# Kernel optimization log

Hardware: AMD Instinct MI355X
Metric: run time of the kernel (lower is better)

## Reference

```python
import jax, jax.numpy as jnp
import numpy as np

B, S, DIM, H = 2, 2048, 1536, 12
HD = DIM // H  # 128
EPS = 1e-6


def setup_inputs() -> dict:
    key = jax.random.key(0)
    ks = jax.random.split(key, 6)
    x = jax.random.normal(ks[0], (B, S, DIM), dtype=jnp.float32)
    # RoPE rotation as (cos, sin) pairs: shape [S, 1, HD//2, 2]
    inv = 1.0 / (10000.0 ** (np.arange(0, HD, 2, dtype=np.float32) / HD))
    ang = np.arange(S, dtype=np.float32)[:, None] * inv[None, :]  # [S, HD//2]
    freqs = jnp.asarray(np.stack([np.cos(ang), np.sin(ang)], axis=-1))[:, None, :, :]
    def lin(k):
        return jax.random.normal(k, (DIM, DIM), dtype=jnp.float32) * 0.02
    wq, wk, wv, wo = lin(ks[1]), lin(ks[2]), lin(ks[3]), lin(ks[4])
    zb = jnp.zeros((DIM,), dtype=jnp.float32)
    ones = jnp.ones((DIM,), dtype=jnp.float32)
    return dict(x=x, freqs=freqs,
                wq=wq, bq=zb, wk=wk, bk=zb, wv=wv, bv=zb, wo=wo, bo=zb,
                gq=ones, gk=ones, timestep=500)


def reference(x, freqs, wq, bq, wk, bk, wv, bv, wo, bo, gq, gk, timestep):
    b, s, dim = x.shape

    def rms(z, g):
        zf = z.astype(jnp.float32)
        n = zf * jax.lax.rsqrt(jnp.mean(zf * zf, axis=-1, keepdims=True) + EPS)
        return n.astype(z.dtype) * g

    def rope(t):
        # [b,s,dim] -> [b,s,H,HD//2,2] pairs; complex multiply by freqs
        tp = t.reshape(b, s, H, HD // 2, 2)
        tr, ti = tp[..., 0], tp[..., 1]
        fr = freqs[None, ..., 0]  # [1,s,1,HD//2] broadcasts over batch & heads
        fi = freqs[None, ..., 1]
        out = jnp.stack([tr * fr - ti * fi, tr * fi + ti * fr], axis=-1)
        return out.reshape(b, s, dim)

    q = rope(rms(x @ wq.T + bq, gq))
    k = rope(rms(x @ wk.T + bk, gk))
    v = x @ wv.T + bv

    qh = q.reshape(b, s, H, HD).transpose(0, 2, 1, 3)
    kh = k.reshape(b, s, H, HD).transpose(0, 2, 1, 3)
    vh = v.reshape(b, s, H, HD).transpose(0, 2, 1, 3)
    scores = jnp.einsum('bhqd,bhkd->bhqk', qh, kh) / np.float32(np.sqrt(HD))
    attn = jax.nn.softmax(scores, axis=-1)
    out = jnp.einsum('bhqk,bhkd->bhqd', attn, vh)
    out = out.transpose(0, 2, 1, 3).reshape(b, s, dim)
    return out @ wo.T + bo
```

## Files before the change

kernel.cpp:

```cpp
#include <hip/hip_runtime.h>
#include <hip/hip_bf16.h>


#define BQ  2
#define SQ  2048
#define DIMQ 1536
#define HQ  12
#define HDQ 128
#define MTOK 4096
#define KDIM 1536

typedef __attribute__((ext_vector_type(8))) short short8;
typedef __attribute__((ext_vector_type(4))) float f32x4;
typedef __attribute__((ext_vector_type(16))) float f32x16;
typedef __attribute__((ext_vector_type(8))) unsigned short u16x8;

typedef __attribute__((address_space(1))) const void global_cvoid;
typedef __attribute__((address_space(3))) void lds_void;

__device__ __forceinline__ float bf2f(unsigned int u) {
    return __uint_as_float(u << 16);
}
__device__ __forceinline__ unsigned short f2bf(float f) {
    unsigned int u = __float_as_uint(f);
    u += 0x7fffu + ((u >> 16) & 1u);
    return (unsigned short)(u >> 16);
}
__device__ __forceinline__ void gload_lds16(const void* g, void* l) {
    __builtin_amdgcn_global_load_lds((global_cvoid*)g, (lds_void*)l, 16, 0, 0);
}
__device__ __forceinline__ unsigned int cvtpk_bf16(float lo, float hi) {
    unsigned int r;
    asm("v_cvt_pk_bf16_f32 %0, %1, %2" : "=v"(r) : "v"(lo), "v"(hi));
    return r;
}

#define VMCNT(n) asm volatile("s_waitcnt vmcnt(" #n ")" ::: "memory")
#define MEMFENCE() asm volatile("" ::: "memory")
#define BARRIER() do { asm volatile("" ::: "memory"); \
                       __builtin_amdgcn_s_barrier();  \
                       asm volatile("" ::: "memory"); } while (0)

__global__ __launch_bounds__(256)
void cast_all(const float* __restrict__ x,
              const float* __restrict__ wq, const float* __restrict__ wk,
              const float* __restrict__ wv, const float* __restrict__ wo,
              unsigned short* __restrict__ Xb,
              unsigned short* __restrict__ Wqkv,
              unsigned short* __restrict__ Wob)
{
    const int NX = 1572864, NW = 589824;
    int i = blockIdx.x * blockDim.x + threadIdx.x;
    int stride = gridDim.x * blockDim.x;
    for (; i < NX + 4 * NW; i += stride) {
        const float* s; unsigned short* d; int off;
        if (i < NX) { s = x; d = Xb; off = i; }
        else {
            int j = i - NX;
            int seg = j / NW;
            off = j - seg * NW;
            s = (seg == 0) ? wq : (seg == 1) ? wk : (seg == 2) ? wv : wo;
            d = (seg < 3) ? (Wqkv + seg * 2359296) : Wob;
        }
        float4 v = ((const float4*)s)[off];
        unsigned short a = f2bf(v.x), b = f2bf(v.y), c = f2bf(v.z), e = f2bf(v.w);
        unsigned int lo = (unsigned int)a | ((unsigned int)b << 16);
        unsigned int hi = (unsigned int)c | ((unsigned int)e << 16);
        ((uint2*)d)[off] = make_uint2(lo, hi);
    }
}

template<int MODE>
__global__ __launch_bounds__(256)
void gemm_bt(const unsigned short* __restrict__ A,
             const unsigned short* __restrict__ Bm,
             unsigned short* __restrict__ oQ,
             unsigned short* __restrict__ oK,
             unsigned short* __restrict__ oV,
             const float* __restrict__ biasq,
             const float* __restrict__ biask,
             const float* __restrict__ biasv,
             float* __restrict__ oF,
             const float* __restrict__ biaso)
{
    __shared__ char smem[32768];
    const int m0 = blockIdx.x * 128;
    const int n0 = blockIdx.y * 128;
    const int t = threadIdx.x;
    const int lane = t & 63;
    const int wid = t >> 6;
    const int wr = (wid >> 1) * 64;
    const int wc = (wid & 1) * 64;
    const int lr = lane & 15;
    const int lk = lane >> 4;

    f32x4 acc[4][4] = {};

    #pragma unroll
    for (int i = 0; i < 2; ++i) {
        const int off = i * 4096 + wid * 1024 + lane * 16;
        const int r = off >> 6;
        const int c = (off >> 4) & 3;
        const int csw = (c ^ (r & 3)) << 3;
        gload_lds16(A + (size_t)(m0 + r) * KDIM + csw,
                    smem + i * 4096 + wid * 1024);
        gload_lds16(Bm + (size_t)(n0 + r) * KDIM + csw,
                    smem + 16384 + i * 4096 + wid * 1024);
    }

    #pragma unroll 1
    for (int s = 0; s < KDIM / 32; ++s) {
        const int cb = s & 1;
        if (s + 1 < KDIM / 32) {
            const int kt = (s + 1) * 32;
            #pragma unroll
            for (int i = 0; i < 2; ++i) {
                const int off = i * 4096 + wid * 1024 + lane * 16;
                const int r = off >> 6;
                const int c = (off >> 4) & 3;
                const int csw = (c ^ (r & 3)) << 3;
                gload_lds16(A + (size_t)(m0 + r) * KDIM + kt + csw,
                            smem + (cb ^ 1) * 8192 + i * 4096 + wid * 1024);
                gload_lds16(Bm + (size_t)(n0 + r) * KDIM + kt + csw,
                            smem + 16384 + (cb ^ 1) * 8192 + i * 4096 + wid * 1024);
            }
            VMCNT(4);
        } else {
            VMCNT(0);
        }
        BARRIER();

        short8 af[4], bf[4];
        #pragma unroll
        for (int mi = 0; mi < 4; ++mi) {
            int row = wr + mi * 16 + lr;
            int ch = lk ^ (row & 3);
            af[mi] = *(const short8*)(smem + cb * 8192 + row * 64 + ch * 16);
        }
        #pragma unroll
        for (int ni = 0; ni < 4; ++ni) {
            int row = wc + ni * 16 + lr;
            int ch = lk ^ (row & 3);
            bf[ni] = *(const short8*)(smem + 16384 + cb * 8192 + row * 64 + ch * 16);
        }
        #pragma unroll
        for (int mi = 0; mi < 4; ++mi)
            #pragma unroll
            for (int ni = 0; ni < 4; ++ni)
                acc[mi][ni] = __builtin_amdgcn_mfma_f32_16x16x32_bf16(
                    af[mi], bf[ni], acc[mi][ni], 0, 0, 0);

        BARRIER();
    }

    if (MODE == 0) {
        const int seg = n0 / 1536;
        const int nl0 = n0 - seg * 1536;
        if (seg < 2) {
            unsigned short* op = (seg == 0) ? oQ : oK;
            const float* bp = (seg == 0) ? biasq : biask;
            #pragma unroll
            for (int mi = 0; mi < 4; ++mi)
                #pragma unroll
                for (int ni = 0; ni < 4; ++ni)
                    #pragma unroll
                    for (int j = 0; j < 4; ++j) {
                        int row = m0 + wr + mi * 16 + lk * 4 + j;
                        int col = nl0 + wc + ni * 16 + lr;
                        op[(size_t)row * 1536 + col] = f2bf(acc[mi][ni][j] + bp[col]);
                    }
        } else {
            #pragma unroll
            for (int mi = 0; mi < 4; ++mi)
                #pragma unroll
                for (int ni = 0; ni < 4; ++ni)
                    #pragma unroll
                    for (int j = 0; j < 4; ++j) {
                        int sl = wr + mi * 16 + lk * 4 + j;
                        int dl = wc + ni * 16 + lr;
                        unsigned short val = f2bf(acc[mi][ni][j] + biasv[nl0 + dl]);
                        *(unsigned short*)(smem + dl * 256 +
                            ((((sl >> 3) ^ (dl & 15))) << 4) + (sl & 7) * 2) = val;
                    }
            BARRIER();
            const int h = nl0 >> 7;
            const int bb = m0 >> 11;
            const int sseq0 = m0 & 2047;
            const int bh = bb * HQ + h;
            #pragma unroll
            for (int p = 0; p < 8; ++p) {
                int d = wid * 32 + p * 4 + lk;
                int sc = lr;
                u16x8 v = *(const u16x8*)(smem + d * 256 + ((sc ^ (d & 15)) << 4));
                *(u16x8*)(oV + (size_t)(bh * HDQ + d) * SQ + sseq0 + sc * 8) = v;
            }
        }
    } else {
        #pragma unroll
        for (int mi = 0; mi < 4; ++mi)
            #pragma unroll
            for (int ni = 0; ni < 4; ++ni)
                #pragma unroll
                for (int j = 0; j < 4; ++j) {
                    int row = m0 + wr + mi * 16 + lk * 4 + j;
                    int col = n0 + wc + ni * 16 + lr;
                    oF[(size_t)row * 1536 + col] = acc[mi][ni][j] + biaso[col];
                }
    }
}

__global__ __launch_bounds__(256)
void rmsnorm_rope(unsigned short* __restrict__ Qb,
                  unsigned short* __restrict__ Kb,
                  const float* __restrict__ gq,
                  const float* __restrict__ gk,
                  const float* __restrict__ freqs)
{
    unsigned short* T = blockIdx.y ? Kb : Qb;
    const float* g = blockIdx.y ? gk : gq;
    const int token = blockIdx.x;
    const int s = token & (SQ - 1);
    unsigned int* row = (unsigned int*)(T + (size_t)token * DIMQ);
    const int t = threadIdx.x;
    const int lane = t & 63, wid = t >> 6;

    float pr[3], pi[3];
    float ss = 0.f;
    #pragma unroll
    for (int q = 0; q < 3; ++q) {
        unsigned int v = row[t + q * 256];
        float a = bf2f(v & 0xffffu);
        float b = bf2f(v >> 16);
        pr[q] = a; pi[q] = b;
        ss += a * a + b * b;
    }
    ss += __shfl_xor(ss, 32); ss += __shfl_xor(ss, 16); ss += __shfl_xor(ss, 8);
    ss += __shfl_xor(ss, 4);  ss += __shfl_xor(ss, 2);  ss += __shfl_xor(ss, 1);
    __shared__ float red[4];
    if (lane == 0) red[wid] = ss;
    __syncthreads();
    float tot = red[0] + red[1] + red[2] + red[3];
    float sc = rsqrtf(tot * (1.0f / 1536.0f) + 1e-6f);

    #pragma unroll
    for (int q = 0; q < 3; ++q) {
        int p = t + q * 256;
        int ph = p & 63;
        float fr = freqs[s * 128 + ph * 2];
        float fi = freqs[s * 128 + ph * 2 + 1];
        float nr = pr[q] * sc * g[2 * p];
        float ni = pi[q] * sc * g[2 * p + 1];
        float outr = nr * fr - ni * fi;
        float outi = nr * fi + ni * fr;
        row[p] = (unsigned int)f2bf(outr) | ((unsigned int)f2bf(outi) << 16);
    }
}

__global__ __launch_bounds__(64, 2)
void attn(const unsigned short* __restrict__ Q,
          const unsigned short* __restrict__ Kb,
          const unsigned short* __restrict__ Vt,
          unsigned short* __restrict__ Ao)
{
    __shared__ char smem[24576];
    char* Kl0 = smem;
    char* Kl1 = smem + 8192;
    char* Vl  = smem + 16384;

    const int fid = blockIdx.x;
    const int xcd = fid & 7;
    const int slot = fid >> 3;
    const int bh = xcd * 3 + (slot >> 6);
    const int sblk = slot & 63;
    const int b = bh / HQ, h = bh % HQ;
    const int s0 = sblk * 32;

    const int lane = threadIdx.x;
    const int l31 = lane & 31, hi = lane >> 5;
    const float CE = 0.12751879f;
    const float THR = 90.5f;

    const unsigned short* Kbase = Kb + (size_t)(b * SQ) * DIMQ + h * HDQ;
    const unsigned short* Vbase = Vt + (size_t)(bh * HDQ) * SQ;

    short8 qf[8];
    {
        const unsigned short* qp = Q + (size_t)(b * SQ + s0 + l31) * DIMQ + h * HDQ;
        #pragma unroll
        for (int kc = 0; kc < 8; ++kc)
            qf[kc] = *(const short8*)(qp + kc * 16 + hi * 8);
    }
    MEMFENCE();
    #pragma unroll
    for (int i = 0; i < 8; ++i) {
        const int off = i * 1024 + lane * 16;
        int r = off >> 8, c = (off >> 4) & 15;
        gload_lds16(Kbase + (size_t)r * DIMQ + ((c ^ (r & 7)) << 3), Kl0 + i * 1024);
    }
    VMCNT(8);

    char* kcur = Kl0;
    char* knxt = Kl1;
    float mrun = -1e30f, lsum = 0.f, nm = 1e30f;
    f32x16 oacc[4] = {};

    #pragma unroll 1
    for (int kv0 = 0; kv0 < SQ; kv0 += 32) {
        #pragma unroll
        for (int i = 0; i < 8; ++i) {
            const int off = i * 1024 + lane * 16;
            int r = off >> 6, c = (off >> 4) & 3;
            gload_lds16(Vbase + (size_t)r * SQ + kv0 + ((c ^ ((r >> 1) & 3)) << 3),
                        Vl + i * 1024);
        }
        MEMFENCE();
        const int kvn = (kv0 + 32 < SQ) ? kv0 + 32 : kv0;
        #pragma unroll
        for (int i = 0; i < 8; ++i) {
            const int off = i * 1024 + lane * 16;
            int r = off >> 8, c = (off >> 4) & 15;
            gload_lds16(Kbase + (size_t)(kvn + r) * DIMQ + ((c ^ (r & 7)) << 3),
                        knxt + i * 1024);
        }

        VMCNT(16);

        f32x16 sa = {}, sb = {};
        const int rb = l31 * 256;
        const int rx = l31 & 7;
        #pragma unroll
        for (int kc = 0; kc < 4; ++kc) {
            short8 kf = *(const short8*)(kcur + rb + (((kc * 2 + hi) ^ rx) << 4));
            sa = __builtin_amdgcn_mfma_f32_32x32x16_bf16(kf, qf[kc], sa, 0, 0, 0);
        }
        #pragma unroll
        for (int kc = 4; kc < 8; ++kc) {
            short8 kf = *(const short8*)(kcur + rb + (((kc * 2 + hi) ^ rx) << 4));
            sb = __builtin_amdgcn_mfma_f32_32x32x16_bf16(kf, qf[kc], sb, 0, 0, 0);
        }
        f32x16 s;
        #pragma unroll
        for (int r = 0; r < 16; ++r) s[r] = sa[r] + sb[r];

        float mt[8];
        #pragma unroll
        for (int r = 0; r < 8; ++r) mt[r] = fmaxf(s[r], s[r + 8]);
        #pragma unroll
        for (int st = 4; st > 0; st >>= 1)
            #pragma unroll
            for (int r = 0; r < 4; ++r)
                if (r < st) mt[r] = fmaxf(mt[r], mt[r + st]);
        float tm = fmaxf(mt[0], __shfl_xor(mt[0], 32));
        if (!__all(tm <= mrun + THR)) {
            float mnew = fmaxf(mrun, tm);
            float al = __builtin_amdgcn_exp2f((mrun - mnew) * CE);
            lsum *= al;
            #pragma unroll
            for (int dt = 0; dt < 4; ++dt)
                #pragma unroll
                for (int r = 0; r < 16; ++r) oacc[dt][r] *= al;
            mrun = mnew;
            nm = -mrun * CE;
        }
        float rs = 0.f;
        #pragma unroll
        for (int r = 0; r < 16; ++r) {
            float p = __builtin_amdgcn_exp2f(__builtin_fmaf(s[r], CE, nm));
            s[r] = p; rs += p;
        }
        rs += __shfl_xor(rs, 32);
        lsum += rs;

        unsigned int A0 = cvtpk_bf16(s[0], s[1]),  A1 = cvtpk_bf16(s[2], s[3]);
        unsigned int B0 = cvtpk_bf16(s[4], s[5]),  B1 = cvtpk_bf16(s[6], s[7]);
        unsigned int C0 = cvtpk_bf16(s[8], s[9]),  C1 = cvtpk_bf16(s[10], s[11]);
        unsigned int D0 = cvtpk_bf16(s[12], s[13]), D1 = cvtpk_bf16(s[14], s[15]);
        unsigned int xA0 = __shfl_xor(A0, 32), xA1 = __shfl_xor(A1, 32);
        unsigned int xB0 = __shfl_xor(B0, 32), xB1 = __shfl_xor(B1, 32);
        unsigned int xC0 = __shfl_xor(C0, 32), xC1 = __shfl_xor(C1, 32);
        unsigned int xD0 = __shfl_xor(D0, 32), xD1 = __shfl_xor(D1, 32);
        union { unsigned int w[4]; short8 v; } pf0, pf1;
        pf0.w[0] = hi ? xB0 : A0;  pf0.w[1] = hi ? xB1 : A1;
        pf0.w[2] = hi ? B0 : xA0;  pf0.w[3] = hi ? B1 : xA1;
        pf1.w[0] = hi ? xD0 : C0;  pf1.w[1] = hi ? xD1 : C1;
        pf1.w[2] = hi ? D0 : xC0;  pf1.w[3] = hi ? D1 : xC1;

        VMCNT(8);

        #pragma unroll
        for (int dt = 0; dt < 4; ++dt) {
            const int drow = dt * 32 + l31;
            const int sw = (drow >> 1) & 3;
            short8 v0 = *(const short8*)(Vl + drow * 64 + ((hi ^ sw) << 4));
            short8 v1 = *(const short8*)(Vl + drow * 64 + (((2 + hi) ^ sw) << 4));
            oacc[dt] = __builtin_amdgcn_mfma_f32_32x32x16_bf16(v0, pf0.v, oacc[dt], 0, 0, 0);
            oacc[dt] = __builtin_amdgcn_mfma_f32_32x32x16_bf16(v1, pf1.v, oacc[dt], 0, 0, 0);
        }

        char* tp = kcur; kcur = knxt; knxt = tp;
    }

    const float rls = 1.0f / lsum;
    char* Ot = Vl;
    #pragma unroll
    for (int dt = 0; dt < 4; ++dt)
        #pragma unroll
        for (int rp = 0; rp < 8; ++rp) {
            const int r = 2 * rp;
            float v0 = oacc[dt][r] * rls;
            float v1 = oacc[dt][r + 1] * rls;
            int d = dt * 32 + (r & 3) + 8 * (r >> 2) + 4 * hi;
            unsigned int w = (unsigned int)f2bf(v0) | ((unsigned int)f2bf(v1) << 16);
            int addr = l31 * 256 + (((d >> 3) ^ (l31 & 7)) << 4) + (d & 7) * 2;
            *(unsigned int*)(Ot + addr) = w;
        }
    #pragma unroll
    for (int ii = 0; ii < 8; ++ii) {
        int task = ii * 64 + lane;
        int q = task >> 4, c = task & 15;
        u16x8 vv = *(const u16x8*)(Ot + q * 256 + ((c ^ (q & 7)) << 4));
        int tok = b * SQ + s0 + q;
        *(u16x8*)(Ao + (size_t)tok * DIMQ + h * HDQ + c * 8) = vv;
    }
}

extern "C" void kernel_launch(void* const* d_in, const int* in_sizes, int n_in,
                              void* d_out, int out_size, void* d_ws, size_t ws_size,
                              hipStream_t stream) {
    (void)in_sizes; (void)n_in; (void)out_size; (void)ws_size;
    const float* x     = (const float*)d_in[0];
    const float* freqs = (const float*)d_in[1];
    const float* wq = (const float*)d_in[2];
    const float* bq = (const float*)d_in[3];
    const float* wk = (const float*)d_in[4];
    const float* bk = (const float*)d_in[5];
    const float* wv = (const float*)d_in[6];
    const float* bv = (const float*)d_in[7];
    const float* wo = (const float*)d_in[8];
    const float* bo = (const float*)d_in[9];
    const float* gq = (const float*)d_in[10];
    const float* gk = (const float*)d_in[11];
    float* out = (float*)d_out;

    char* w = (char*)d_ws;
    unsigned short* Xb   = (unsigned short*)(w);
    unsigned short* Wqkv = (unsigned short*)(w + 12582912);
    unsigned short* Wob  = (unsigned short*)(w + 26738688);
    unsigned short* Qb   = (unsigned short*)(w + 31457280);
    unsigned short* Kbuf = (unsigned short*)(w + 44040192);
    unsigned short* Vt   = (unsigned short*)(w + 69206016);
    unsigned short* Ao   = Xb;

    cast_all<<<2048, 256, 0, stream>>>(x, wq, wk, wv, wo, Xb, Wqkv, Wob);

    gemm_bt<0><<<dim3(32, 36), 256, 0, stream>>>(
        Xb, Wqkv, Qb, Kbuf, Vt, bq, bk, bv, nullptr, nullptr);

    rmsnorm_rope<<<dim3(4096, 2), 256, 0, stream>>>(Qb, Kbuf, gq, gk, freqs);

    attn<<<1536, 64, 0, stream>>>(Qb, Kbuf, Vt, Ao);

    gemm_bt<1><<<dim3(32, 12), 256, 0, stream>>>(
        Ao, Wob, nullptr, nullptr, nullptr, nullptr, nullptr, nullptr, out, bo);
}
```

Before: 236.1 us.

## Split attention KV range in two with combine kernel and shared K/V LDS buffer

Splits each query tile's KV sweep into two halves (flash-decoding style), doubling the attention grid to 3072 single-wave blocks. Each half writes normalized partial outputs plus running max and sum, and a new combine kernel merges them with softmax rescaling. The LDS footprint drops to 16 KB by loading V into the current K buffer after the QK MFMAs and prefetching K two tiles ahead. The goal is more parallelism and occupancy per CU. The cost is an extra kernel launch, workspace traffic for the partials, and a bf16 rounding of the partial outputs.

Measured after the change: 238.3 us. Within noise of the previous version (+0.9%).

```diff
diff --git a/kernel.cpp b/kernel.cpp
--- a/kernel.cpp
+++ b/kernel.cpp
@@ -18,6 +18,8 @@
 typedef __attribute__((address_space(1))) const void global_cvoid;
 typedef __attribute__((address_space(3))) void lds_void;
 
+__device__ const float CEc = 0.12751879f;
+
 __device__ __forceinline__ float bf2f(unsigned int u) {
     return __uint_as_float(u << 16);
 }
@@ -36,6 +38,7 @@
 }
 
 #define VMCNT(n) asm volatile("s_waitcnt vmcnt(" #n ")" ::: "memory")
+#define LGKMCNT0() asm volatile("s_waitcnt lgkmcnt(0)" ::: "memory")
 #define MEMFENCE() asm volatile("" ::: "memory")
 #define BARRIER() do { asm volatile("" ::: "memory"); \
                        __builtin_amdgcn_s_barrier();  \
@@ -260,24 +263,26 @@
 void attn(const unsigned short* __restrict__ Q,
           const unsigned short* __restrict__ Kb,
           const unsigned short* __restrict__ Vt,
-          unsigned short* __restrict__ Ao)
+          unsigned short* __restrict__ Op0,
+          unsigned short* __restrict__ Op1,
+          float* __restrict__ ml)
 {
-    __shared__ char smem[24576];
-    char* Kl0 = smem;
-    char* Kl1 = smem + 8192;
-    char* Vl  = smem + 16384;
+    __shared__ char smem[16384];
 
     const int fid = blockIdx.x;
     const int xcd = fid & 7;
     const int slot = fid >> 3;
-    const int bh = xcd * 3 + (slot >> 6);
-    const int sblk = slot & 63;
+    const int bh = xcd * 3 + (slot >> 7);
+    const int rem = slot & 127;
+    const int qtile = rem >> 1;
+    const int sp = rem & 1;
     const int b = bh / HQ, h = bh % HQ;
-    const int s0 = sblk * 32;
+    const int s0 = qtile * 32;
+    const int f = bh * 64 + qtile;
+    const int kvbeg = sp * 1024;
 
     const int lane = threadIdx.x;
     const int l31 = lane & 31, hi = lane >> 5;
-    const float CE = 0.12751879f;
     const float THR = 90.5f;
 
     const unsigned short* Kbase = Kb + (size_t)(b * SQ) * DIMQ + h * HDQ;
@@ -295,52 +300,54 @@
     for (int i = 0; i < 8; ++i) {
         const int off = i * 1024 + lane * 16;
         int r = off >> 8, c = (off >> 4) & 15;
-        gload_lds16(Kbase + (size_t)r * DIMQ + ((c ^ (r & 7)) << 3), Kl0 + i * 1024);
+        gload_lds16(Kbase + (size_t)(kvbeg + r) * DIMQ + ((c ^ (r & 7)) << 3),
+                    smem + i * 1024);
+    }
+    MEMFENCE();
+    #pragma unroll
+    for (int i = 0; i < 8; ++i) {
+        const int off = i * 1024 + lane * 16;
+        int r = off >> 8, c = (off >> 4) & 15;
+        gload_lds16(Kbase + (size_t)(kvbeg + 32 + r) * DIMQ + ((c ^ (r & 7)) << 3),
+                    smem + 8192 + i * 1024);
     }
     VMCNT(8);
 
-    char* kcur = Kl0;
-    char* knxt = Kl1;
+    char* kcur = smem;
+    char* knxt = smem + 8192;
     float mrun = -1e30f, lsum = 0.f, nm = 1e30f;
     f32x16 oacc[4] = {};
 
     #pragma unroll 1
-    for (int kv0 = 0; kv0 < SQ; kv0 += 32) {
+    for (int t = 0; t < 32; ++t) {
+        const int kv0 = kvbeg + t * 32;
+
+        f32x16 sa = {}, sb = {};
+        const int rb = l31 * 256;
+        const int rx = l31 & 7;
+        #pragma unroll
+        for (int kc = 0; kc < 4; ++kc) {
+            short8 kf = *(const short8*)(kcur + rb + (((kc * 2 + hi) ^ rx) << 4));
+            sa = __builtin_amdgcn_mfma_f32_32x32x16_bf16(kf, qf[kc], sa, 0, 0, 0);
+        }
+        #pragma unroll
+        for (int kc = 4; kc < 8; ++kc) {
+            short8 kf = *(const short8*)(kcur + rb + (((kc * 2 + hi) ^ rx) << 4));
+            sb = __builtin_amdgcn_mfma_f32_32x32x16_bf16(kf, qf[kc], sb, 0, 0, 0);
+        }
+        f32x16 s;
+        #pragma unroll
+        for (int r = 0; r < 16; ++r) s[r] = sa[r] + sb[r];
+
+        asm volatile("" :: "v"(s[0]) : "memory");
+
         #pragma unroll
         for (int i = 0; i < 8; ++i) {
             const int off = i * 1024 + lane * 16;
             int r = off >> 6, c = (off >> 4) & 3;
             gload_lds16(Vbase + (size_t)r * SQ + kv0 + ((c ^ ((r >> 1) & 3)) << 3),
-                        Vl + i * 1024);
-        }
-        MEMFENCE();
-        const int kvn = (kv0 + 32 < SQ) ? kv0 + 32 : kv0;
-        #pragma unroll
-        for (int i = 0; i < 8; ++i) {
-            const int off = i * 1024 + lane * 16;
-            int r = off >> 8, c = (off >> 4) & 15;
-            gload_lds16(Kbase + (size_t)(kvn + r) * DIMQ + ((c ^ (r & 7)) << 3),
-                        knxt + i * 1024);
-        }
-
-        VMCNT(16);
-
-        f32x16 sa = {}, sb = {};
-        const int rb = l31 * 256;
-        const int rx = l31 & 7;
-        #pragma unroll
-        for (int kc = 0; kc < 4; ++kc) {
-            short8 kf = *(const short8*)(kcur + rb + (((kc * 2 + hi) ^ rx) << 4));
-            sa = __builtin_amdgcn_mfma_f32_32x32x16_bf16(kf, qf[kc], sa, 0, 0, 0);
-        }
-        #pragma unroll
-        for (int kc = 4; kc < 8; ++kc) {
-            short8 kf = *(const short8*)(kcur + rb + (((kc * 2 + hi) ^ rx) << 4));
-            sb = __builtin_amdgcn_mfma_f32_32x32x16_bf16(kf, qf[kc], sb, 0, 0, 0);
-        }
-        f32x16 s;
-        #pragma unroll
-        for (int r = 0; r < 16; ++r) s[r] = sa[r] + sb[r];
+                        kcur + i * 1024);
+        }
 
         float mt[8];
         #pragma unroll
@@ -353,19 +360,19 @@
         float tm = fmaxf(mt[0], __shfl_xor(mt[0], 32));
         if (!__all(tm <= mrun + THR)) {
             float mnew = fmaxf(mrun, tm);
-            float al = __builtin_amdgcn_exp2f((mrun - mnew) * CE);
+            float al = __builtin_amdgcn_exp2f((mrun - mnew) * CEc);
             lsum *= al;
             #pragma unroll
             for (int dt = 0; dt < 4; ++dt)
                 #pragma unroll
                 for (int r = 0; r < 16; ++r) oacc[dt][r] *= al;
             mrun = mnew;
-            nm = -mrun * CE;
+            nm = -mrun * CEc;
         }
         float rs = 0.f;
         #pragma unroll
         for (int r = 0; r < 16; ++r) {
-            float p = __builtin_amdgcn_exp2f(__builtin_fmaf(s[r], CE, nm));
+            float p = __builtin_amdgcn_exp2f(__builtin_fmaf(s[r], CEc, nm));
             s[r] = p; rs += p;
         }
         rs += __shfl_xor(rs, 32);
@@ -385,41 +392,98 @@
         pf1.w[0] = hi ? xD0 : C0;  pf1.w[1] = hi ? xD1 : C1;
         pf1.w[2] = hi ? D0 : xC0;  pf1.w[3] = hi ? D1 : xC1;
 
-        VMCNT(8);
+        VMCNT(0);
 
         #pragma unroll
         for (int dt = 0; dt < 4; ++dt) {
             const int drow = dt * 32 + l31;
             const int sw = (drow >> 1) & 3;
-            short8 v0 = *(const short8*)(Vl + drow * 64 + ((hi ^ sw) << 4));
-            short8 v1 = *(const short8*)(Vl + drow * 64 + (((2 + hi) ^ sw) << 4));
+            short8 v0 = *(const short8*)(kcur + drow * 64 + ((hi ^ sw) << 4));
+            short8 v1 = *(const short8*)(kcur + drow * 64 + (((2 + hi) ^ sw) << 4));
             oacc[dt] = __builtin_amdgcn_mfma_f32_32x32x16_bf16(v0, pf0.v, oacc[dt], 0, 0, 0);
             oacc[dt] = __builtin_amdgcn_mfma_f32_32x32x16_bf16(v1, pf1.v, oacc[dt], 0, 0, 0);
         }
 
+        LGKMCNT0();
+
+        if (t + 2 < 32) {
+            #pragma unroll
+            for (int i = 0; i < 8; ++i) {
+                const int off = i * 1024 + lane * 16;
+                int r = off >> 8, c = (off >> 4) & 15;
+                gload_lds16(Kbase + (size_t)(kv0 + 64 + r) * DIMQ + ((c ^ (r & 7)) << 3),
+                            kcur + i * 1024);
+            }
+        }
+
         char* tp = kcur; kcur = knxt; knxt = tp;
     }
 
-    const float rls = 1.0f / lsum;
-    char* Ot = Vl;
+    float rnl = 1.0f / lsum;
+    unsigned short* Op = sp ? Op1 : Op0;
+    #pragma unroll
+    for (int dt = 0; dt < 4; ++dt) {
+        unsigned int w[8];
+        #pragma unroll
+        for (int j = 0; j < 8; ++j)
+            w[j] = (unsigned int)f2bf(oacc[dt][2 * j] * rnl)
+                 | ((unsigned int)f2bf(oacc[dt][2 * j + 1] * rnl) << 16);
+        *(uint4*)(Op + (size_t)f * 4096 + (dt * 2 + 0) * 512 + lane * 8) =
+            make_uint4(w[0], w[1], w[2], w[3]);
+        *(uint4*)(Op + (size_t)f * 4096 + (dt * 2 + 1) * 512 + lane * 8) =
+            make_uint4(w[4], w[5], w[6], w[7]);
+    }
+    ml[(size_t)(sp * 1536 + f) * 128 + lane] = mrun;
+    ml[(size_t)(sp * 1536 + f) * 128 + 64 + lane] = lsum;
+}
+
+__global__ __launch_bounds__(256)
+void attn_combine(const unsigned short* __restrict__ Op0,
+                  const unsigned short* __restrict__ Op1,
+                  const float* __restrict__ ml,
+                  unsigned short* __restrict__ Ao)
+{
+    __shared__ char smem[32768];
+    const int f = blockIdx.x * 4 + (threadIdx.x >> 6);
+    const int lane = threadIdx.x & 63;
+    const int l31 = lane & 31, hi = lane >> 5;
+    const int bh = f >> 6;
+    const int b = bh / HQ, h = bh % HQ;
+    const int s0q = (f & 63) * 32;
+
+    float m0 = ml[(size_t)f * 128 + lane];
+    float l0 = ml[(size_t)f * 128 + 64 + lane];
+    float m1 = ml[(size_t)(1536 + f) * 128 + lane];
+    float l1 = ml[(size_t)(1536 + f) * 128 + 64 + lane];
+    float ms = fmaxf(m0, m1);
+    float w0 = __builtin_amdgcn_exp2f((m0 - ms) * CEc) * l0;
+    float w1 = __builtin_amdgcn_exp2f((m1 - ms) * CEc) * l1;
+    float rL = 1.0f / (w0 + w1);
+    float a0 = w0 * rL, a1 = w1 * rL;
+
+    char* Ot = smem + (threadIdx.x >> 6) * 8192;
     #pragma unroll
     for (int dt = 0; dt < 4; ++dt)
         #pragma unroll
-        for (int rp = 0; rp < 8; ++rp) {
-            const int r = 2 * rp;
-            float v0 = oacc[dt][r] * rls;
-            float v1 = oacc[dt][r + 1] * rls;
-            int d = dt * 32 + (r & 3) + 8 * (r >> 2) + 4 * hi;
-            unsigned int w = (unsigned int)f2bf(v0) | ((unsigned int)f2bf(v1) << 16);
-            int addr = l31 * 256 + (((d >> 3) ^ (l31 & 7)) << 4) + (d & 7) * 2;
-            *(unsigned int*)(Ot + addr) = w;
+        for (int hf = 0; hf < 2; ++hf) {
+            u16x8 o0 = *(const u16x8*)(Op0 + (size_t)f * 4096 + (dt * 2 + hf) * 512 + lane * 8);
+            u16x8 o1 = *(const u16x8*)(Op1 + (size_t)f * 4096 + (dt * 2 + hf) * 512 + lane * 8);
+            #pragma unroll
+            for (int j = 0; j < 4; ++j) {
+                int r = hf * 8 + 2 * j;
+                float v0 = a0 * bf2f((unsigned short)o0[2 * j])     + a1 * bf2f((unsigned short)o1[2 * j]);
+                float v1 = a0 * bf2f((unsigned short)o0[2 * j + 1]) + a1 * bf2f((unsigned short)o1[2 * j + 1]);
+                int d = dt * 32 + (r & 3) + 8 * (r >> 2) + 4 * hi;
+                unsigned int w = (unsigned int)f2bf(v0) | ((unsigned int)f2bf(v1) << 16);
+                *(unsigned int*)(Ot + l31 * 256 + (((d >> 3) ^ (l31 & 7)) << 4) + (d & 7) * 2) = w;
+            }
         }
     #pragma unroll
     for (int ii = 0; ii < 8; ++ii) {
         int task = ii * 64 + lane;
         int q = task >> 4, c = task & 15;
         u16x8 vv = *(const u16x8*)(Ot + q * 256 + ((c ^ (q & 7)) << 4));
-        int tok = b * SQ + s0 + q;
+        int tok = b * SQ + s0q + q;
         *(u16x8*)(Ao + (size_t)tok * DIMQ + h * HDQ + c * 8) = vv;
     }
 }
@@ -450,6 +514,9 @@
     unsigned short* Kbuf = (unsigned short*)(w + 44040192);
     unsigned short* Vt   = (unsigned short*)(w + 69206016);
     unsigned short* Ao   = Xb;
+    unsigned short* Op0  = Wqkv;
+    float*          mlbf = (float*)(w + 25165824);
+    unsigned short* Op1  = (unsigned short*)(w + 56623104);
 
     cast_all<<<2048, 256, 0, stream>>>(x, wq, wk, wv, wo, Xb, Wqkv, Wob);
 
@@ -458,7 +525,8 @@
 
     rmsnorm_rope<<<dim3(4096, 2), 256, 0, stream>>>(Qb, Kbuf, gq, gk, freqs);
 
-    attn<<<1536, 64, 0, stream>>>(Qb, Kbuf, Vt, Ao);
+    attn<<<3072, 64, 0, stream>>>(Qb, Kbuf, Vt, Op0, Op1, mlbf);
+    attn_combine<<<384, 256, 0, stream>>>(Op0, Op1, mlbf, Ao);
 
     gemm_bt<1><<<dim3(32, 12), 256, 0, stream>>>(
         Ao, Wob, nullptr, nullptr, nullptr, nullptr, nullptr, nullptr, out, bo);
```
